# Kernel optimization log

Hardware: AMD Instinct MI355X
Metric: run time of the kernel (lower is better)

The kernel has to match this reference:

```python
import jax, jax.numpy as jnp
import numpy as np

N, D = 8192, 256

def setup_inputs() -> dict:
    key = jax.random.key(0)
    k1, k2 = jax.random.split(key)
    data = jnp.zeros((1,), dtype=jnp.float32)  # unused by the module
    Z = jax.random.normal(k1, (N, D), dtype=jnp.float32)
    A_hat = jax.random.uniform(k2, (N, N), dtype=jnp.float32)
    return {"data": data, "Z": Z, "A_hat": A_hat}

def reference(data, Z, A_hat):
    A = A_hat.astype(jnp.float32)
    # D^{-1/2} A D^{-1/2}: diagonal matmuls are mathematically row/col scaling
    d_inv_sqrt = 1.0 / jnp.sqrt(A.sum(axis=1) + 1e-10)  # [N]
    A_norm = A * d_inv_sqrt[:, None] * d_inv_sqrt[None, :]  # [N, N]
    # cosine similarity (F.normalize uses eps=1e-12 clamp on the norm)
    z_norm = jnp.linalg.norm(Z, axis=1, keepdims=True)
    Z_n = Z / jnp.maximum(z_norm, 1e-12)
    similarity = Z_n @ Z_n.T  # [N, N]
    homo_loss = -jnp.sum(A_norm * similarity)
    hetero_loss = jnp.sum((1.0 - A_norm) * similarity)
    return (homo_loss, hetero_loss)
```

## Files before the change

kernel.cpp:

```cpp
#include <hip/hip_runtime.h>
#include <hip/hip_fp16.h>

typedef _Float16 f16x4  __attribute__((ext_vector_type(4)));
typedef float    f32x16 __attribute__((ext_vector_type(16)));

constexpr int Nn = 8192;
constexpr int Dd = 256;

constexpr int BM  = 256;
constexpr int KC  = 1024;
constexpr int SK  = 64;
constexpr int NSC = KC / SK;
constexpr int NB  = 4;
constexpr int ABYTES = BM * SK;
constexpr int YBYTES = Dd * SK;

#define AS1 __attribute__((address_space(1)))
#define AS3 __attribute__((address_space(3)))

__global__ __launch_bounds__(256) void k_rowcvt(const float* __restrict__ A,
                                                unsigned char* __restrict__ Af8,
                                                float* __restrict__ dis,
                                                float* __restrict__ rd,
                                                float* __restrict__ s,
                                                float* __restrict__ T) {
    if (blockIdx.x == 0) {
        if (threadIdx.x == 0) *T = 0.f;
        s[threadIdx.x] = 0.f;
    }
    const int row  = blockIdx.x * 4 + (threadIdx.x >> 6);
    const int lane = threadIdx.x & 63;
    const float4*  rp = reinterpret_cast<const float4*>(A + (size_t)row * Nn);
    unsigned int*  wp = reinterpret_cast<unsigned int*>(Af8 + (size_t)row * Nn);
    float sum = 0.f;
    #pragma unroll
    for (int i = 0; i < Nn / 256; ++i) {
        float4 v = rp[i * 64 + lane];
        sum += (v.x + v.y) + (v.z + v.w);
        int p = __builtin_amdgcn_cvt_pk_fp8_f32(v.x, v.y, 0, false);
        p     = __builtin_amdgcn_cvt_pk_fp8_f32(v.z, v.w, p, true);
        wp[i * 64 + lane] = (unsigned int)p;
    }
    #pragma unroll
    for (int off = 32; off > 0; off >>= 1) sum += __shfl_down(sum, off, 64);
    if (lane == 0) {
        float rs = sum + 1e-10f;
        dis[row] = rsqrtf(rs);
        rd[row]  = sqrtf(rs);
    }
}

__global__ __launch_bounds__(256) void k_makeYt(const float* __restrict__ Z,
                                               const float* __restrict__ dis,
                                               unsigned char* __restrict__ Ytf8,
                                               _Float16* __restrict__ Yr) {
    __shared__ float nrm[64][4];
    __shared__ unsigned char tile[Dd][80];
    const int t = threadIdx.x;
    const int r = t >> 2, q = t & 3;
    const int row = blockIdx.x * 64 + r;
    const float4* zp = reinterpret_cast<const float4*>(Z + (size_t)row * Dd + q * 64);
    float4 v[16];
    float ss = 0.f;
    #pragma unroll
    for (int i = 0; i < 16; ++i) {
        v[i] = zp[i];
        ss += v[i].x*v[i].x + v[i].y*v[i].y + v[i].z*v[i].z + v[i].w*v[i].w;
    }
    nrm[r][q] = ss;
    __syncthreads();
    const float tot  = nrm[r][0] + nrm[r][1] + nrm[r][2] + nrm[r][3];
    const float sc   = dis[row] / fmaxf(sqrtf(tot), 1e-12f);
    const float sc8  = 64.f * sc;
    #pragma unroll
    for (int i = 0; i < 16; ++i) {
        const int c0 = q * 64 + i * 4;
        f16x4 y = { (_Float16)(v[i].x * sc), (_Float16)(v[i].y * sc),
                    (_Float16)(v[i].z * sc), (_Float16)(v[i].w * sc) };
        *reinterpret_cast<f16x4*>(Yr + (size_t)row * Dd + c0) = y;
        int p = __builtin_amdgcn_cvt_pk_fp8_f32(v[i].x * sc8, v[i].y * sc8, 0, false);
        p     = __builtin_amdgcn_cvt_pk_fp8_f32(v[i].z * sc8, v[i].w * sc8, p, true);
        tile[c0+0][r] = (unsigned char)(p);
        tile[c0+1][r] = (unsigned char)(p >> 8);
        tile[c0+2][r] = (unsigned char)(p >> 16);
        tile[c0+3][r] = (unsigned char)(p >> 24);
    }
    __syncthreads();
    int4*       dst = reinterpret_cast<int4*>(Ytf8 + (size_t)t * Nn + blockIdx.x * 64);
    const int4* src = reinterpret_cast<const int4*>(&tile[t][0]);
    #pragma unroll
    for (int i = 0; i < 4; ++i) dst[i] = src[i];
}

__global__ __launch_bounds__(256) void k_colsum(const _Float16* __restrict__ Yr,
                                                const float* __restrict__ rd,
                                                float* __restrict__ s) {
    const int c  = threadIdx.x;
    const int r0 = blockIdx.x * 256;
    float acc = 0.f;
    const _Float16* yp = Yr + (size_t)r0 * Dd + c;
    #pragma unroll 8
    for (int r = 0; r < 256; ++r) acc += (float)yp[(size_t)r * Dd] * rd[r0 + r];
    atomicAdd(&s[c], acc);
}

__global__ __launch_bounds__(1024, 4) void k_main(const unsigned char* __restrict__ Af8,
                                                  const unsigned char* __restrict__ Ytf8,
                                                  const _Float16* __restrict__ Yr,
                                                  float* __restrict__ T) {
    __shared__ long As[NB * ABYTES / 8];
    __shared__ long Ys[NB * YBYTES / 8];
    char* As8 = (char*)As;
    char* Ys8 = (char*)Ys;

    const int ib = blockIdx.x & (Nn / BM - 1);
    const int jb = blockIdx.x >> 5;
    const int I0 = ib * BM;
    const int K0 = jb * KC;
    const int t   = threadIdx.x;
    const int w   = t >> 6;
    const int wm  = w >> 1;
    const int wn  = w & 1;
    const int l   = t & 63;
    const int ln  = l & 31;
    const int lkh = l >> 5;

    f32x16 acc[4];
    #pragma unroll
    for (int q = 0; q < 4; ++q) acc[q] = (f32x16)(0.f);

    #define STAGE(SC, B)                                                       \
    {   const int kc = K0 + (SC) * SK;                                         \
        const int rr = w * 16 + (l >> 2);                                      \
        const int sg = ((l & 3) ^ ((rr >> 1) & 3)) * 16;                       \
        __builtin_amdgcn_global_load_lds(                                      \
            (const AS1 unsigned int*)(Af8 + (size_t)(I0 + rr) * Nn + kc + sg), \
            (AS3 unsigned int*)(As8 + (B) * ABYTES + w * 1024), 16, 0, 0);     \
        __builtin_amdgcn_global_load_lds(                                      \
            (const AS1 unsigned int*)(Ytf8 + (size_t)rr * Nn + kc + sg),       \
            (AS3 unsigned int*)(Ys8 + (B) * YBYTES + w * 1024), 16, 0, 0);     \
    }

    #define WAITV(N) asm volatile("s_waitcnt vmcnt(" #N ")" ::: "memory")

    STAGE(0, 0); STAGE(1, 1); STAGE(2, 2);

    for (int sc = 0; sc < NSC; ++sc) {
        const int ah = NSC - 1 - sc;
        if (ah >= 2) WAITV(4); else if (ah == 1) WAITV(2); else WAITV(0);
        __builtin_amdgcn_s_barrier();
        if (sc + 3 < NSC) STAGE(sc + 3, (sc + 3) & 3);

        const int cb = sc & 3;
        const long* Al = reinterpret_cast<const long*>(As8 + cb * ABYTES);
        const long* Yl = reinterpret_cast<const long*>(Ys8 + cb * YBYTES);
        const int r  = wm * 32 + ln;
        const int xA = ((r >> 1) & 3) << 1;
        long af[4];
        #pragma unroll
        for (int ks = 0; ks < 4; ++ks) af[ks] = Al[r * 8 + ((ks * 2 + lkh) ^ xA)];
        #pragma unroll
        for (int tn = 0; tn < 4; ++tn) {
            const int n  = wn * 128 + tn * 32 + ln;
            const int xN = ((n >> 1) & 3) << 1;
            #pragma unroll
            for (int ks = 0; ks < 4; ++ks) {
                const long bf = Yl[n * 8 + ((ks * 2 + lkh) ^ xN)];
                acc[tn] = __builtin_amdgcn_mfma_f32_32x32x16_fp8_fp8(af[ks], bf, acc[tn], 0, 0, 0);
            }
        }
    }

    float part = 0.f;
    #pragma unroll
    for (int tn = 0; tn < 4; ++tn) {
        const int n = wn * 128 + tn * 32 + ln;
        #pragma unroll
        for (int rr = 0; rr < 16; ++rr) {
            const int i = I0 + wm * 32 + (rr & 3) + 8 * (rr >> 2) + 4 * lkh;
            part += acc[tn][rr] * (float)Yr[(size_t)i * Dd + n];
        }
    }
    #pragma unroll
    for (int off = 32; off > 0; off >>= 1) part += __shfl_down(part, off, 64);
    __shared__ float red[16];
    if (l == 0) red[w] = part;
    __syncthreads();
    if (threadIdx.x == 0) {
        float tt = 0.f;
        #pragma unroll
        for (int i = 0; i < 16; ++i) tt += red[i];
        atomicAdd(T, tt * 0.015625f);
    }
}

__global__ __launch_bounds__(256) void k_final(const float* __restrict__ s,
                                               const float* __restrict__ T,
                                               float* __restrict__ out) {
    const int t = threadIdx.x;
    float v = s[t];
    float p = v * v;
    #pragma unroll
    for (int off = 32; off > 0; off >>= 1) p += __shfl_down(p, off, 64);
    __shared__ float red[4];
    if ((t & 63) == 0) red[t >> 6] = p;
    __syncthreads();
    if (t == 0) {
        const float ss = red[0] + red[1] + red[2] + red[3];
        const float Tv = *T;
        out[0] = -Tv;
        out[1] = ss - Tv;
    }
}

extern "C" void kernel_launch(void* const* d_in, const int* in_sizes, int n_in,
                              void* d_out, int out_size, void* d_ws, size_t ws_size,
                              hipStream_t stream) {
    const float* Z = (const float*)d_in[1];
    const float* A = (const float*)d_in[2];
    float* out = (float*)d_out;

    char* ws = (char*)d_ws;
    float*         dis  = (float*)(ws);
    float*         rd   = (float*)(ws + 32768);
    float*         s    = (float*)(ws + 65536);
    float*         T    = (float*)(ws + 66560);
    _Float16*      Yr   = (_Float16*)(ws + 131072);
    unsigned char* Ytf8 = (unsigned char*)(ws + 131072 + (size_t)Nn * Dd * 2);
    unsigned char* Af8  = (unsigned char*)(ws + 131072 + (size_t)Nn * Dd * 3);

    k_rowcvt<<<Nn / 4, 256, 0, stream>>>(A, Af8, dis, rd, s, T);
    k_makeYt<<<Nn / 64, 256, 0, stream>>>(Z, dis, Ytf8, Yr);
    k_colsum<<<Nn / 256, 256, 0, stream>>>(Yr, rd, s);
    k_main<<<(Nn / BM) * (Nn / KC), 1024, 0, stream>>>(Af8, Ytf8, Yr, T);
    k_final<<<1, 256, 0, stream>>>(s, T, out);
}
```

Baseline: 126.9 us.

## Fuse all stages into one cooperative kernel with grid sync

Replaces the five-kernel pipeline with a single cooperative kernel. Each block converts its 32 rows of A to fp8, builds the scaled Z rows and the column sums, then waits on a grid-wide sync before running the fp8 MFMA stage. A last-block counter handles the final reduction. This removes four launch gaps and the separate colsum and final kernels. In exchange it adds grid-sync cost and relies on all 256 blocks of 1024 threads being co-resident, with the old launch path kept as a fallback if the cooperative launch fails.

```diff
diff --git a/kernel.cpp b/kernel.cpp
--- a/kernel.cpp
+++ b/kernel.cpp
@@ -1,5 +1,8 @@
 #include <hip/hip_runtime.h>
 #include <hip/hip_fp16.h>
+#include <hip/hip_cooperative_groups.h>
+
+namespace cg = cooperative_groups;
 
 typedef _Float16 f16x4  __attribute__((ext_vector_type(4)));
 typedef float    f32x16 __attribute__((ext_vector_type(16)));
@@ -17,6 +20,193 @@
 
 #define AS1 __attribute__((address_space(1)))
 #define AS3 __attribute__((address_space(3)))
+#define WAITV(N) asm volatile("s_waitcnt vmcnt(" #N ")" ::: "memory")
+
+__global__ __launch_bounds__(1024, 4) void k_mega(
+    const float* __restrict__ A, const float* __restrict__ Z,
+    unsigned char* __restrict__ Af8, unsigned char* __restrict__ Ytf8,
+    _Float16* __restrict__ Yr, float* __restrict__ s,
+    float* __restrict__ T, unsigned int* __restrict__ cnt,
+    float* __restrict__ out)
+{
+    __shared__ long SM[16384];
+    __shared__ int  islast;
+    char* smem = (char*)SM;
+    unsigned char (*tile)[40] = (unsigned char(*)[40])smem;
+    float* sacc = (float*)(smem + 10496);
+    float* disL = (float*)(smem + 11776);
+    float* rdL  = (float*)(smem + 11904);
+    float* red  = (float*)smem;
+
+    const int b = blockIdx.x;
+    const int t = threadIdx.x;
+    const int w = t >> 6;
+    const int l = t & 63;
+
+    if (t < 256) sacc[t] = 0.f;
+    if (b == 0) {
+        if (t == 0) { *T = 0.f; *cnt = 0u; }
+        if (t < 256) s[t] = 0.f;
+    }
+    __syncthreads();
+
+    #pragma unroll
+    for (int h = 0; h < 2; ++h) {
+        const int row = b * 32 + w * 2 + h;
+        const float4* rp = reinterpret_cast<const float4*>(A + (size_t)row * Nn);
+        unsigned int* wp = reinterpret_cast<unsigned int*>(Af8 + (size_t)row * Nn);
+        float sum = 0.f;
+        #pragma unroll 4
+        for (int i = 0; i < 32; ++i) {
+            float4 v = rp[i * 64 + l];
+            sum += (v.x + v.y) + (v.z + v.w);
+            int p = __builtin_amdgcn_cvt_pk_fp8_f32(v.x, v.y, 0, false);
+            p     = __builtin_amdgcn_cvt_pk_fp8_f32(v.z, v.w, p, true);
+            wp[i * 64 + l] = (unsigned int)p;
+        }
+        #pragma unroll
+        for (int off = 32; off > 0; off >>= 1) sum += __shfl_down(sum, off, 64);
+        if (l == 0) {
+            float rs = sum + 1e-10f;
+            disL[w * 2 + h] = rsqrtf(rs);
+            rdL [w * 2 + h] = sqrtf(rs);
+        }
+    }
+
+    #pragma unroll
+    for (int h = 0; h < 2; ++h) {
+        const int lr  = w * 2 + h;
+        const int row = b * 32 + lr;
+        float4 v = reinterpret_cast<const float4*>(Z + (size_t)row * Dd)[l];
+        float ss = v.x*v.x + v.y*v.y + v.z*v.z + v.w*v.w;
+        #pragma unroll
+        for (int off = 32; off > 0; off >>= 1) ss += __shfl_down(ss, off, 64);
+        ss = __shfl(ss, 0, 64);
+        const float dis = disL[lr], rd = rdL[lr];
+        const float sc  = dis / fmaxf(sqrtf(ss), 1e-12f);
+        const float sc8 = 64.f * sc;
+        const float y0 = v.x*sc, y1 = v.y*sc, y2 = v.z*sc, y3 = v.w*sc;
+        *reinterpret_cast<f16x4*>(Yr + (size_t)row * Dd + l * 4) =
+            f16x4{ (_Float16)y0, (_Float16)y1, (_Float16)y2, (_Float16)y3 };
+        int p = __builtin_amdgcn_cvt_pk_fp8_f32(v.x*sc8, v.y*sc8, 0, false);
+        p     = __builtin_amdgcn_cvt_pk_fp8_f32(v.z*sc8, v.w*sc8, p, true);
+        tile[l*4+0][lr] = (unsigned char)(p);
+        tile[l*4+1][lr] = (unsigned char)(p >> 8);
+        tile[l*4+2][lr] = (unsigned char)(p >> 16);
+        tile[l*4+3][lr] = (unsigned char)(p >> 24);
+        atomicAdd(&sacc[l*4+0], rd * y0);
+        atomicAdd(&sacc[l*4+1], rd * y1);
+        atomicAdd(&sacc[l*4+2], rd * y2);
+        atomicAdd(&sacc[l*4+3], rd * y3);
+    }
+    __syncthreads();
+    {
+        const int n = t >> 2, sg = (t & 3) * 8;
+        *reinterpret_cast<long*>(Ytf8 + (size_t)n * Nn + b * 32 + sg) =
+            *reinterpret_cast<const long*>(&tile[n][sg]);
+    }
+
+    __threadfence();
+    cg::this_grid().sync();
+    WAITV(0);
+    if (t < 256) atomicAdd(&s[t], sacc[t]);
+    WAITV(0);
+    __syncthreads();
+
+    char* As8 = smem;
+    char* Ys8 = smem + 65536;
+    const int ib = b & 31, jb = b >> 5;
+    const int I0 = ib * BM, K0 = jb * KC;
+    const int wm = w >> 1, wn = w & 1;
+    const int ln = l & 31, lkh = l >> 5;
+
+    f32x16 acc[4];
+    #pragma unroll
+    for (int q = 0; q < 4; ++q) acc[q] = (f32x16)(0.f);
+
+    #define STAGE(SC, B)                                                       \
+    {   const int kc = K0 + (SC) * SK;                                         \
+        const int rr = w * 16 + (l >> 2);                                      \
+        const int sg = ((l & 3) ^ ((rr >> 1) & 3)) * 16;                       \
+        __builtin_amdgcn_global_load_lds(                                      \
+            (const AS1 unsigned int*)(Af8 + (size_t)(I0 + rr) * Nn + kc + sg), \
+            (AS3 unsigned int*)(As8 + (B) * ABYTES + w * 1024), 16, 0, 0);     \
+        __builtin_amdgcn_global_load_lds(                                      \
+            (const AS1 unsigned int*)(Ytf8 + (size_t)rr * Nn + kc + sg),       \
+            (AS3 unsigned int*)(Ys8 + (B) * YBYTES + w * 1024), 16, 0, 0);     \
+    }
+
+    STAGE(0, 0); STAGE(1, 1); STAGE(2, 2);
+
+    for (int sc = 0; sc < NSC; ++sc) {
+        const int ah = NSC - 1 - sc;
+        if (ah >= 2) WAITV(4); else if (ah == 1) WAITV(2); else WAITV(0);
+        __builtin_amdgcn_s_barrier();
+        if (sc + 3 < NSC) STAGE(sc + 3, (sc + 3) & 3);
+
+        const int cb = sc & 3;
+        const long* Al = reinterpret_cast<const long*>(As8 + cb * ABYTES);
+        const long* Yl = reinterpret_cast<const long*>(Ys8 + cb * YBYTES);
+        const int r  = wm * 32 + ln;
+        const int xA = ((r >> 1) & 3) << 1;
+        long af[4];
+        #pragma unroll
+        for (int ks = 0; ks < 4; ++ks) af[ks] = Al[r * 8 + ((ks * 2 + lkh) ^ xA)];
+        #pragma unroll
+        for (int tn = 0; tn < 4; ++tn) {
+            const int n  = wn * 128 + tn * 32 + ln;
+            const int xN = ((n >> 1) & 3) << 1;
+            #pragma unroll
+            for (int ks = 0; ks < 4; ++ks) {
+                const long bf = Yl[n * 8 + ((ks * 2 + lkh) ^ xN)];
+                acc[tn] = __builtin_amdgcn_mfma_f32_32x32x16_fp8_fp8(af[ks], bf, acc[tn], 0, 0, 0);
+            }
+        }
+    }
+    #undef STAGE
+
+    float part = 0.f;
+    #pragma unroll
+    for (int tn = 0; tn < 4; ++tn) {
+        const int n = wn * 128 + tn * 32 + ln;
+        #pragma unroll
+        for (int rr = 0; rr < 16; ++rr) {
+            const int i = I0 + wm * 32 + (rr & 3) + 8 * (rr >> 2) + 4 * lkh;
+            part += acc[tn][rr] * (float)Yr[(size_t)i * Dd + n];
+        }
+    }
+    #pragma unroll
+    for (int off = 32; off > 0; off >>= 1) part += __shfl_down(part, off, 64);
+    if (l == 0) red[w] = part;
+    __syncthreads();
+    if (t == 0) {
+        float tt = 0.f;
+        #pragma unroll
+        for (int i = 0; i < 16; ++i) tt += red[i];
+        atomicAdd(T, tt * 0.015625f);
+    }
+
+    __threadfence();
+    if (t == 0) islast = (atomicAdd(cnt, 1u) == 255u) ? 1 : 0;
+    __syncthreads();
+    if (islast) {
+        float p = 0.f;
+        if (t < 256) { float sv = atomicAdd(&s[t], 0.f); p = sv * sv; }
+        #pragma unroll
+        for (int off = 32; off > 0; off >>= 1) p += __shfl_down(p, off, 64);
+        __syncthreads();
+        if (l == 0) red[w] = p;
+        __syncthreads();
+        if (t == 0) {
+            float ss = 0.f;
+            #pragma unroll
+            for (int i = 0; i < 16; ++i) ss += red[i];
+            const float Tv = atomicAdd(T, 0.f);
+            out[0] = -Tv;
+            out[1] = ss - Tv;
+        }
+    }
+}
 
 __global__ __launch_bounds__(256) void k_rowcvt(const float* __restrict__ A,
                                                 unsigned char* __restrict__ Af8,
@@ -129,7 +319,7 @@
     #pragma unroll
     for (int q = 0; q < 4; ++q) acc[q] = (f32x16)(0.f);
 
-    #define STAGE(SC, B)                                                       \
+    #define STAGEF(SC, B)                                                      \
     {   const int kc = K0 + (SC) * SK;                                         \
         const int rr = w * 16 + (l >> 2);                                      \
         const int sg = ((l & 3) ^ ((rr >> 1) & 3)) * 16;                       \
@@ -141,15 +331,13 @@
             (AS3 unsigned int*)(Ys8 + (B) * YBYTES + w * 1024), 16, 0, 0);     \
     }
 
-    #define WAITV(N) asm volatile("s_waitcnt vmcnt(" #N ")" ::: "memory")
-
-    STAGE(0, 0); STAGE(1, 1); STAGE(2, 2);
+    STAGEF(0, 0); STAGEF(1, 1); STAGEF(2, 2);
 
     for (int sc = 0; sc < NSC; ++sc) {
         const int ah = NSC - 1 - sc;
         if (ah >= 2) WAITV(4); else if (ah == 1) WAITV(2); else WAITV(0);
         __builtin_amdgcn_s_barrier();
-        if (sc + 3 < NSC) STAGE(sc + 3, (sc + 3) & 3);
+        if (sc + 3 < NSC) STAGEF(sc + 3, (sc + 3) & 3);
 
         const int cb = sc & 3;
         const long* Al = reinterpret_cast<const long*>(As8 + cb * ABYTES);
@@ -170,6 +358,7 @@
             }
         }
     }
+    #undef STAGEF
 
     float part = 0.f;
     #pragma unroll
@@ -225,13 +414,21 @@
     float*         rd   = (float*)(ws + 32768);
     float*         s    = (float*)(ws + 65536);
     float*         T    = (float*)(ws + 66560);
+    unsigned int*  cnt  = (unsigned int*)(ws + 66564);
     _Float16*      Yr   = (_Float16*)(ws + 131072);
     unsigned char* Ytf8 = (unsigned char*)(ws + 131072 + (size_t)Nn * Dd * 2);
     unsigned char* Af8  = (unsigned char*)(ws + 131072 + (size_t)Nn * Dd * 3);
 
-    k_rowcvt<<<Nn / 4, 256, 0, stream>>>(A, Af8, dis, rd, s, T);
-    k_makeYt<<<Nn / 64, 256, 0, stream>>>(Z, dis, Ytf8, Yr);
-    k_colsum<<<Nn / 256, 256, 0, stream>>>(Yr, rd, s);
-    k_main<<<(Nn / BM) * (Nn / KC), 1024, 0, stream>>>(Af8, Ytf8, Yr, T);
-    k_final<<<1, 256, 0, stream>>>(s, T, out);
-}
+    void* args[] = { (void*)&A, (void*)&Z, (void*)&Af8, (void*)&Ytf8,
+                     (void*)&Yr, (void*)&s, (void*)&T, (void*)&cnt, (void*)&out };
+    hipError_t err = hipLaunchCooperativeKernel((const void*)k_mega,
+                                                dim3(256), dim3(1024),
+                                                args, 0, stream);
+    if (err != hipSuccess) {
+        k_rowcvt<<<Nn / 4, 256, 0, stream>>>(A, Af8, dis, rd, s, T);
+        k_makeYt<<<Nn / 64, 256, 0, stream>>>(Z, dis, Ytf8, Yr);
+        k_colsum<<<Nn / 256, 256, 0, stream>>>(Yr, rd, s);
+        k_main<<<(Nn / BM) * (Nn / KC), 1024, 0, stream>>>(Af8, Ytf8, Yr, T);
+        k_final<<<1, 256, 0, stream>>>(s, T, out);
+    }
+}
```

Measured after the change: 326.6 us. 157% more time.

## Halve main-kernel tile rows, double-buffer LDS, fold final reduction into last block

Applied to the files above, without the earlier changes.

The main fp8 MFMA kernel now uses 128-row tiles with 512 threads, which doubles the grid to 512 blocks. It cuts the LDS ring from four buffers to two, with a full vmcnt(0) wait each step, to lower LDS use and raise occupancy. The separate k_final launch is removed: the last block to finish, found through an atomic counter, computes the output. This drops one launch but makes each block load Y tiles more often and gives less prefetch depth to hide latency.

```diff
diff --git a/kernel.cpp b/kernel.cpp
--- a/kernel.cpp
+++ b/kernel.cpp
@@ -7,25 +7,26 @@
 constexpr int Nn = 8192;
 constexpr int Dd = 256;
 
-constexpr int BM  = 256;
+constexpr int BM  = 128;
 constexpr int KC  = 1024;
 constexpr int SK  = 64;
 constexpr int NSC = KC / SK;
-constexpr int NB  = 4;
 constexpr int ABYTES = BM * SK;
 constexpr int YBYTES = Dd * SK;
 
 #define AS1 __attribute__((address_space(1)))
 #define AS3 __attribute__((address_space(3)))
+#define WAITV(N) asm volatile("s_waitcnt vmcnt(" #N ")" ::: "memory")
 
 __global__ __launch_bounds__(256) void k_rowcvt(const float* __restrict__ A,
                                                 unsigned char* __restrict__ Af8,
                                                 float* __restrict__ dis,
                                                 float* __restrict__ rd,
                                                 float* __restrict__ s,
-                                                float* __restrict__ T) {
+                                                float* __restrict__ T,
+                                                unsigned int* __restrict__ cnt) {
     if (blockIdx.x == 0) {
-        if (threadIdx.x == 0) *T = 0.f;
+        if (threadIdx.x == 0) { *T = 0.f; *cnt = 0u; }
         s[threadIdx.x] = 0.f;
     }
     const int row  = blockIdx.x * 4 + (threadIdx.x >> 6);
@@ -104,17 +105,20 @@
     atomicAdd(&s[c], acc);
 }
 
-__global__ __launch_bounds__(1024, 4) void k_main(const unsigned char* __restrict__ Af8,
-                                                  const unsigned char* __restrict__ Ytf8,
-                                                  const _Float16* __restrict__ Yr,
-                                                  float* __restrict__ T) {
-    __shared__ long As[NB * ABYTES / 8];
-    __shared__ long Ys[NB * YBYTES / 8];
-    char* As8 = (char*)As;
-    char* Ys8 = (char*)Ys;
-
-    const int ib = blockIdx.x & (Nn / BM - 1);
-    const int jb = blockIdx.x >> 5;
+__global__ __launch_bounds__(512, 4) void k_main(const unsigned char* __restrict__ Af8,
+                                                 const unsigned char* __restrict__ Ytf8,
+                                                 const _Float16* __restrict__ Yr,
+                                                 const float* __restrict__ s,
+                                                 float* __restrict__ T,
+                                                 unsigned int* __restrict__ cnt,
+                                                 float* __restrict__ out) {
+    __shared__ char As8[2 * ABYTES];
+    __shared__ char Ys8[2 * YBYTES];
+    __shared__ float red[8];
+    __shared__ int islast;
+
+    const int ib = blockIdx.x & 63;
+    const int jb = blockIdx.x >> 6;
     const int I0 = ib * BM;
     const int K0 = jb * KC;
     const int t   = threadIdx.x;
@@ -131,27 +135,31 @@
 
     #define STAGE(SC, B)                                                       \
     {   const int kc = K0 + (SC) * SK;                                         \
-        const int rr = w * 16 + (l >> 2);                                      \
-        const int sg = ((l & 3) ^ ((rr >> 1) & 3)) * 16;                       \
-        __builtin_amdgcn_global_load_lds(                                      \
-            (const AS1 unsigned int*)(Af8 + (size_t)(I0 + rr) * Nn + kc + sg), \
-            (AS3 unsigned int*)(As8 + (B) * ABYTES + w * 1024), 16, 0, 0);     \
-        __builtin_amdgcn_global_load_lds(                                      \
-            (const AS1 unsigned int*)(Ytf8 + (size_t)rr * Nn + kc + sg),       \
-            (AS3 unsigned int*)(Ys8 + (B) * YBYTES + w * 1024), 16, 0, 0);     \
-    }
-
-    #define WAITV(N) asm volatile("s_waitcnt vmcnt(" #N ")" ::: "memory")
-
-    STAGE(0, 0); STAGE(1, 1); STAGE(2, 2);
+        {   const int rr = w * 16 + (l >> 2);                                  \
+            const int sg = ((l & 3) ^ ((rr >> 1) & 3)) * 16;                   \
+            __builtin_amdgcn_global_load_lds(                                  \
+                (const AS1 unsigned int*)(Af8 + (size_t)(I0 + rr) * Nn + kc + sg), \
+                (AS3 unsigned int*)(As8 + (B) * ABYTES + w * 1024), 16, 0, 0); \
+        }                                                                      \
+        _Pragma("unroll")                                                      \
+        for (int q2 = 0; q2 < 2; ++q2) {                                       \
+            const int nr = w * 32 + q2 * 16 + (l >> 2);                        \
+            const int sg = ((l & 3) ^ ((nr >> 1) & 3)) * 16;                   \
+            __builtin_amdgcn_global_load_lds(                                  \
+                (const AS1 unsigned int*)(Ytf8 + (size_t)nr * Nn + kc + sg),   \
+                (AS3 unsigned int*)(Ys8 + (B) * YBYTES + (w * 32 + q2 * 16) * 64), \
+                16, 0, 0);                                                     \
+        }                                                                      \
+    }
+
+    STAGE(0, 0);
 
     for (int sc = 0; sc < NSC; ++sc) {
-        const int ah = NSC - 1 - sc;
-        if (ah >= 2) WAITV(4); else if (ah == 1) WAITV(2); else WAITV(0);
+        WAITV(0);
         __builtin_amdgcn_s_barrier();
-        if (sc + 3 < NSC) STAGE(sc + 3, (sc + 3) & 3);
-
-        const int cb = sc & 3;
+        if (sc + 1 < NSC) STAGE(sc + 1, (sc + 1) & 1);
+
+        const int cb = sc & 1;
         const long* Al = reinterpret_cast<const long*>(As8 + cb * ABYTES);
         const long* Yl = reinterpret_cast<const long*>(Ys8 + cb * YBYTES);
         const int r  = wm * 32 + ln;
@@ -170,6 +178,7 @@
             }
         }
     }
+    #undef STAGE
 
     float part = 0.f;
     #pragma unroll
@@ -183,33 +192,33 @@
     }
     #pragma unroll
     for (int off = 32; off > 0; off >>= 1) part += __shfl_down(part, off, 64);
-    __shared__ float red[16];
     if (l == 0) red[w] = part;
     __syncthreads();
-    if (threadIdx.x == 0) {
+    if (t == 0) {
         float tt = 0.f;
         #pragma unroll
-        for (int i = 0; i < 16; ++i) tt += red[i];
+        for (int i = 0; i < 8; ++i) tt += red[i];
         atomicAdd(T, tt * 0.015625f);
     }
-}
-
-__global__ __launch_bounds__(256) void k_final(const float* __restrict__ s,
-                                               const float* __restrict__ T,
-                                               float* __restrict__ out) {
-    const int t = threadIdx.x;
-    float v = s[t];
-    float p = v * v;
-    #pragma unroll
-    for (int off = 32; off > 0; off >>= 1) p += __shfl_down(p, off, 64);
-    __shared__ float red[4];
-    if ((t & 63) == 0) red[t >> 6] = p;
-    __syncthreads();
-    if (t == 0) {
-        const float ss = red[0] + red[1] + red[2] + red[3];
-        const float Tv = *T;
-        out[0] = -Tv;
-        out[1] = ss - Tv;
+
+    __threadfence();
+    if (t == 0) islast = (atomicAdd(cnt, 1u) == (unsigned)(gridDim.x - 1)) ? 1 : 0;
+    __syncthreads();
+    if (islast) {
+        float p = 0.f;
+        if (t < 256) { const float sv = s[t]; p = sv * sv; }
+        #pragma unroll
+        for (int off = 32; off > 0; off >>= 1) p += __shfl_down(p, off, 64);
+        if (l == 0) red[w] = p;
+        __syncthreads();
+        if (t == 0) {
+            float ss = 0.f;
+            #pragma unroll
+            for (int i = 0; i < 8; ++i) ss += red[i];
+            const float Tv = atomicAdd(T, 0.f);
+            out[0] = -Tv;
+            out[1] = ss - Tv;
+        }
     }
 }
 
@@ -225,13 +234,13 @@
     float*         rd   = (float*)(ws + 32768);
     float*         s    = (float*)(ws + 65536);
     float*         T    = (float*)(ws + 66560);
+    unsigned int*  cnt  = (unsigned int*)(ws + 66564);
     _Float16*      Yr   = (_Float16*)(ws + 131072);
     unsigned char* Ytf8 = (unsigned char*)(ws + 131072 + (size_t)Nn * Dd * 2);
     unsigned char* Af8  = (unsigned char*)(ws + 131072 + (size_t)Nn * Dd * 3);
 
-    k_rowcvt<<<Nn / 4, 256, 0, stream>>>(A, Af8, dis, rd, s, T);
+    k_rowcvt<<<Nn / 4, 256, 0, stream>>>(A, Af8, dis, rd, s, T, cnt);
     k_makeYt<<<Nn / 64, 256, 0, stream>>>(Z, dis, Ytf8, Yr);
     k_colsum<<<Nn / 256, 256, 0, stream>>>(Yr, rd, s);
-    k_main<<<(Nn / BM) * (Nn / KC), 1024, 0, stream>>>(Af8, Ytf8, Yr, T);
-    k_final<<<1, 256, 0, stream>>>(s, T, out);
-}
+    k_main<<<(Nn / BM) * (Nn / KC), 512, 0, stream>>>(Af8, Ytf8, Yr, s, T, cnt, out);
+}
```

After: 188.1 us. 1.48x slower.
